# Kernel optimization log

Measured on AMD Instinct MI355X. Metric: run time of the kernel, lower is better.

The kernel has to match this reference:

```python
import jax, jax.numpy as jnp
import numpy as np

B, C, H, W = 16, 512, 32, 32
G = 32            # GroupNorm groups (hard-coded in Normalize)
EPS = 1e-6
TEXT = 180        # text_ch
F = H * W         # in_features, asserted H*W == in_features


def setup_inputs() -> dict:
    key = jax.random.key(0)
    ks = jax.random.split(key, 10)
    s = 0.02
    return {
        "x": jax.random.normal(ks[0], (B, C, H, W), dtype=jnp.float32),
        "condition": jax.random.normal(ks[1], (B, TEXT), dtype=jnp.float32),
        "gamma": jnp.ones((C,), dtype=jnp.float32),
        "beta": jnp.zeros((C,), dtype=jnp.float32),
        "wq": jax.random.normal(ks[2], (C, C), dtype=jnp.float32) * s,   # 1x1 conv [out,in]
        "bq": jax.random.normal(ks[3], (C,), dtype=jnp.float32) * s,
        "wk": jax.random.normal(ks[4], (F, TEXT), dtype=jnp.float32) * s,  # Linear(text_ch -> in_features)
        "bk": jax.random.normal(ks[5], (F,), dtype=jnp.float32) * s,
        "wv": jax.random.normal(ks[6], (F, TEXT), dtype=jnp.float32) * s,
        "bv": jax.random.normal(ks[7], (F,), dtype=jnp.float32) * s,
        "wo": jax.random.normal(ks[8], (C, C), dtype=jnp.float32) * s,   # proj_out 1x1 conv
        "bo": jax.random.normal(ks[9], (C,), dtype=jnp.float32) * s,
    }


def _group_norm(x, gamma, beta):
    b, c, h, w = x.shape
    xg = x.reshape(b, G, c // G, h, w)
    mu = xg.mean(axis=(2, 3, 4), keepdims=True)
    var = xg.var(axis=(2, 3, 4), keepdims=True)
    xn = ((xg - mu) * jax.lax.rsqrt(var + EPS)).reshape(b, c, h, w)
    return xn * gamma[None, :, None, None] + beta[None, :, None, None]


def reference(x, condition, gamma, beta, wq, bq, wk, bk, wv, bv, wo, bo):
    h_ = _group_norm(x, gamma, beta)                       # [B,C,H,W]
    # q: 1x1 conv
    q = jnp.einsum('bchw,oc->bohw', h_, wq) + bq[None, :, None, None]
    # condition.reshape(B,1,-1).repeat(1,C,1)
    cond = jnp.broadcast_to(condition[:, None, :], (B, C, TEXT))  # [B,C,T]
    k = jnp.einsum('bct,ft->bcf', cond, wk) + bk           # [B,C,F]
    v = jnp.einsum('bct,ft->bcf', cond, wv) + bv           # [B,C,F]
    q3 = q.reshape(B, C, H * W).transpose(0, 2, 1)         # [B,N,C], N=HW
    scale = C ** (-0.5)
    attn = jax.nn.softmax(jnp.einsum('bnc,bcf->bnf', q3, k) * scale, axis=2)  # [B,N,F]
    h2 = jnp.einsum('bcf,bnf->bcn', v, attn).reshape(B, C, H, W)
    out = jnp.einsum('bchw,oc->bohw', h2, wo) + bo[None, :, None, None]
    return x + out
```

## Files before the change

### kernel.cpp

```cpp
#include <hip/hip_runtime.h>

#define B_   16
#define C_   512
#define N_   1024
#define F_   1024
#define T_   180
#define G_   32

#define WS_MU    0
#define WS_RSIG  512
#define WS_K     1024
#define WS_V     (1024 + 16384)
#define WS_WQS   (1024 + 2*16384)
#define WS_WOS   (WS_WQS + 512)
#define WS_BQS   (WS_WOS + 512)

__global__ __launch_bounds__(256) void k_prep(
    const float* __restrict__ x, const float* __restrict__ cond,
    const float* __restrict__ wq, const float* __restrict__ bq,
    const float* __restrict__ wk, const float* __restrict__ bk,
    const float* __restrict__ wv, const float* __restrict__ bv,
    const float* __restrict__ wo, float* __restrict__ ws)
{
    const int blk = blockIdx.x;
    const int tid = threadIdx.x;

    if (blk < 512) {
        const float4* xv = (const float4*)(x + (size_t)blk * 16384);
        float s = 0.f, sq = 0.f;
        #pragma unroll
        for (int j = 0; j < 16; ++j) {
            float4 p = xv[tid + (j << 8)];
            s  += (p.x + p.y) + (p.z + p.w);
            sq += p.x * p.x + p.y * p.y + p.z * p.z + p.w * p.w;
        }
        #pragma unroll
        for (int off = 32; off; off >>= 1) {
            s  += __shfl_down(s,  off, 64);
            sq += __shfl_down(sq, off, 64);
        }
        __shared__ float rs[4], rq[4];
        if ((tid & 63) == 0) { rs[tid >> 6] = s; rq[tid >> 6] = sq; }
        __syncthreads();
        if (tid == 0) {
            float S1 = rs[0] + rs[1] + rs[2] + rs[3];
            float S2 = rq[0] + rq[1] + rq[2] + rq[3];
            float mu = S1 * (1.f / 16384.f);
            float var = S2 * (1.f / 16384.f) - mu * mu;
            ws[WS_MU + blk]   = mu;
            ws[WS_RSIG + blk] = rsqrtf(var + 1e-6f);
        }
    } else if (blk < 576) {
        const int idx = blk - 512;
        const int b   = idx >> 2;
        const int f   = ((idx & 3) << 8) + tid;
        __shared__ float condl[T_];
        if (tid < T_) condl[tid] = cond[b * T_ + tid];
        __syncthreads();
        float accK = bk[f];
        float accV = bv[f];
        const float* wkr = wk + f * T_;
        const float* wvr = wv + f * T_;
        #pragma unroll 4
        for (int t = 0; t < T_; ++t) {
            float cf = condl[t];
            accK += cf * wkr[t];
            accV += cf * wvr[t];
        }
        ws[WS_K + b * F_ + f] = accK;
        ws[WS_V + b * F_ + f] = accV;
    } else if (blk < 578) {
        const int c = ((blk - 576) << 8) + tid;
        float acc = 0.f;
        for (int o = 0; o < C_; ++o) acc += wq[o * C_ + c];
        ws[WS_WQS + c] = acc;
    } else if (blk < 580) {
        const int o = ((blk - 578) << 8) + tid;
        const float4* row = (const float4*)(wo + o * C_);
        float acc = 0.f;
        #pragma unroll 8
        for (int j = 0; j < 128; ++j) {
            float4 p = row[j];
            acc += (p.x + p.y) + (p.z + p.w);
        }
        ws[WS_WOS + o] = acc;
    } else {
        float p = bq[tid] + bq[tid + 256];
        #pragma unroll
        for (int off = 32; off; off >>= 1) p += __shfl_down(p, off, 64);
        __shared__ float rb[4];
        if ((tid & 63) == 0) rb[tid >> 6] = p;
        __syncthreads();
        if (tid == 0) ws[WS_BQS] = rb[0] + rb[1] + rb[2] + rb[3];
    }
}

__global__ __launch_bounds__(256) void k_fused(
    const float* __restrict__ x, const float* __restrict__ gamma,
    const float* __restrict__ beta, const float* __restrict__ bo,
    const float* __restrict__ ws, float* __restrict__ out)
{
    const int b   = blockIdx.x >> 5;
    const int n0  = (blockIdx.x & 31) << 5;
    const int tid = threadIdx.x;

    __shared__ float coef[C_];
    __shared__ float KV[2 * F_];
    __shared__ float part[8][32];
    __shared__ float pse[8][32], psv[8][32];
    __shared__ float Sl[32], Al[32];
    __shared__ float opw[4], redmx[4], redmn[4];

    float op = 0.f;
    #pragma unroll
    for (int c = tid; c < C_; c += 256) {
        const int g = c >> 4;
        float rsig = ws[WS_RSIG + b * G_ + g];
        float mu   = ws[WS_MU   + b * G_ + g];
        float gm   = gamma[c];
        float wqs  = ws[WS_WQS + c];
        coef[c] = rsig * gm * wqs;
        op += (beta[c] - mu * rsig * gm) * wqs;
    }
    const float* Kg = ws + WS_K + b * F_;
    const float* Vg = ws + WS_V + b * F_;
    float mx = -1e30f, mn = 1e30f;
    #pragma unroll
    for (int i = tid; i < F_; i += 256) {
        float kv = Kg[i];
        KV[2 * i]     = kv;
        KV[2 * i + 1] = Vg[i];
        mx = fmaxf(mx, kv);
        mn = fminf(mn, kv);
    }
    #pragma unroll
    for (int off = 32; off; off >>= 1) {
        op += __shfl_down(op, off, 64);
        mx = fmaxf(mx, __shfl_down(mx, off, 64));
        mn = fminf(mn, __shfl_down(mn, off, 64));
    }
    if ((tid & 63) == 0) {
        opw[tid >> 6]   = op;
        redmx[tid >> 6] = mx;
        redmn[tid >> 6] = mn;
    }
    __syncthreads();
    const float offset = ws[WS_BQS] + opw[0] + opw[1] + opw[2] + opw[3];
    const float maxK = fmaxf(fmaxf(redmx[0], redmx[1]), fmaxf(redmx[2], redmx[3]));
    const float minK = fminf(fminf(redmn[0], redmn[1]), fminf(redmn[2], redmn[3]));

    const int nl = tid & 31;
    const int cq = tid >> 5;
    {
        const float* xp = x + (((b * C_ + (cq << 6)) << 10) + n0 + nl);
        float acc = 0.f;
        #pragma unroll 8
        for (int ci = 0; ci < 64; ++ci) {
            acc += xp[ci << 10] * coef[(cq << 6) + ci];
        }
        part[cq][nl] = acc;
    }
    __syncthreads();
    if (tid < 32) {
        float s8 = 0.f;
        #pragma unroll
        for (int j = 0; j < 8; ++j) s8 += part[j][tid];
        Sl[tid] = s8 + offset;
    }
    __syncthreads();

    const float LOG2E = 1.4426950408889634f;
    const float scale = 0.044194173824159216f;
    const float s  = Sl[nl] * scale;
    const float sl = s * LOG2E;
    const float ml = (s >= 0.f ? maxK : minK) * sl;

    float se = 0.f, sv = 0.f;
    const int fq = tid >> 5;
    const int fbase = fq << 7;
    #pragma unroll 8
    for (int fi = 0; fi < 128; ++fi) {
        const int f = fbase + fi;
        float kf = KV[2 * f];
        float vf = KV[2 * f + 1];
        float e = exp2f(fmaf(sl, kf, -ml));
        se += e;
        sv = fmaf(vf, e, sv);
    }
    pse[fq][nl] = se;
    psv[fq][nl] = sv;
    __syncthreads();
    if (tid < 32) {
        float den = 0.f, num = 0.f;
        #pragma unroll
        for (int j = 0; j < 8; ++j) { den += pse[j][tid]; num += psv[j][tid]; }
        Al[tid] = num / den;
    }
    __syncthreads();

    const int col = tid & 7;
    const int row = tid >> 3;
    float av[4];
    #pragma unroll
    for (int j = 0; j < 4; ++j) av[j] = Al[(col << 2) + j];
    const float* WOS = ws + WS_WOS;

    for (int p = 0; p < 16; ++p) {
        const int o = (p << 5) + row;
        const float w   = WOS[o];
        const float bof = bo[o];
        const size_t base = (((size_t)(b * C_ + o)) << 10) + n0 + (col << 2);
        float4 xv = *(const float4*)(x + base);
        float4 ov;
        ov.x = xv.x + fmaf(av[0], w, bof);
        ov.y = xv.y + fmaf(av[1], w, bof);
        ov.z = xv.z + fmaf(av[2], w, bof);
        ov.w = xv.w + fmaf(av[3], w, bof);
        *(float4*)(out + base) = ov;
    }
}

extern "C" void kernel_launch(void* const* d_in, const int* in_sizes, int n_in,
                              void* d_out, int out_size, void* d_ws, size_t ws_size,
                              hipStream_t stream) {
    const float* x     = (const float*)d_in[0];
    const float* cond  = (const float*)d_in[1];
    const float* gamma = (const float*)d_in[2];
    const float* beta  = (const float*)d_in[3];
    const float* wq    = (const float*)d_in[4];
    const float* bq    = (const float*)d_in[5];
    const float* wk    = (const float*)d_in[6];
    const float* bk    = (const float*)d_in[7];
    const float* wv    = (const float*)d_in[8];
    const float* bv    = (const float*)d_in[9];
    const float* wo    = (const float*)d_in[10];
    const float* bo    = (const float*)d_in[11];
    float* ws  = (float*)d_ws;
    float* out = (float*)d_out;

    hipLaunchKernelGGL(k_prep, dim3(581), dim3(256), 0, stream,
                       x, cond, wq, bq, wk, bk, wv, bv, wo, ws);
    hipLaunchKernelGGL(k_fused, dim3(512), dim3(256), 0, stream,
                       x, gamma, beta, bo, ws, out);
}
```

Measured before the change: 138.3 us.

## Fuse group-norm stats with per-group q-projection partial sums in one x pass

The previous flow read x once in the prep kernel for group statistics, again in the fused kernel for the q dot product, and a third time for the residual. Now a new kernel computes group mean/rstd and the weighted channel sum per group in the same read of x, writing per-group partial q values to workspace. The fused kernel then sums 32 group partials instead of re-reading 512 channels of x. It also processes 64 positions per block with fewer blocks. The cost is an extra launch and a serialized dependency: the weight-prep kernel must finish before k_gs, since k_gs reads its column sums of wq.

```diff
diff --git a/kernel.cpp b/kernel.cpp
--- a/kernel.cpp
+++ b/kernel.cpp
@@ -7,16 +7,15 @@
 #define T_   180
 #define G_   32
 
-#define WS_MU    0
-#define WS_RSIG  512
-#define WS_K     1024
-#define WS_V     (1024 + 16384)
-#define WS_WQS   (1024 + 2*16384)
+#define WS_K     0
+#define WS_V     16384
+#define WS_WQS   (2*16384)
 #define WS_WOS   (WS_WQS + 512)
 #define WS_BQS   (WS_WOS + 512)
-
-__global__ __launch_bounds__(256) void k_prep(
-    const float* __restrict__ x, const float* __restrict__ cond,
+#define WS_SG    (WS_BQS + 64)
+
+__global__ __launch_bounds__(256) void k_w(
+    const float* __restrict__ cond,
     const float* __restrict__ wq, const float* __restrict__ bq,
     const float* __restrict__ wk, const float* __restrict__ bk,
     const float* __restrict__ wv, const float* __restrict__ bv,
@@ -25,35 +24,9 @@
     const int blk = blockIdx.x;
     const int tid = threadIdx.x;
 
-    if (blk < 512) {
-        const float4* xv = (const float4*)(x + (size_t)blk * 16384);
-        float s = 0.f, sq = 0.f;
-        #pragma unroll
-        for (int j = 0; j < 16; ++j) {
-            float4 p = xv[tid + (j << 8)];
-            s  += (p.x + p.y) + (p.z + p.w);
-            sq += p.x * p.x + p.y * p.y + p.z * p.z + p.w * p.w;
-        }
-        #pragma unroll
-        for (int off = 32; off; off >>= 1) {
-            s  += __shfl_down(s,  off, 64);
-            sq += __shfl_down(sq, off, 64);
-        }
-        __shared__ float rs[4], rq[4];
-        if ((tid & 63) == 0) { rs[tid >> 6] = s; rq[tid >> 6] = sq; }
-        __syncthreads();
-        if (tid == 0) {
-            float S1 = rs[0] + rs[1] + rs[2] + rs[3];
-            float S2 = rq[0] + rq[1] + rq[2] + rq[3];
-            float mu = S1 * (1.f / 16384.f);
-            float var = S2 * (1.f / 16384.f) - mu * mu;
-            ws[WS_MU + blk]   = mu;
-            ws[WS_RSIG + blk] = rsqrtf(var + 1e-6f);
-        }
-    } else if (blk < 576) {
-        const int idx = blk - 512;
-        const int b   = idx >> 2;
-        const int f   = ((idx & 3) << 8) + tid;
+    if (blk < 64) {
+        const int b = blk >> 2;
+        const int f = ((blk & 3) << 8) + tid;
         __shared__ float condl[T_];
         if (tid < T_) condl[tid] = cond[b * T_ + tid];
         __syncthreads();
@@ -69,13 +42,13 @@
         }
         ws[WS_K + b * F_ + f] = accK;
         ws[WS_V + b * F_ + f] = accV;
-    } else if (blk < 578) {
-        const int c = ((blk - 576) << 8) + tid;
+    } else if (blk < 66) {
+        const int c = ((blk - 64) << 8) + tid;
         float acc = 0.f;
         for (int o = 0; o < C_; ++o) acc += wq[o * C_ + c];
         ws[WS_WQS + c] = acc;
-    } else if (blk < 580) {
-        const int o = ((blk - 578) << 8) + tid;
+    } else if (blk < 68) {
+        const int o = ((blk - 66) << 8) + tid;
         const float4* row = (const float4*)(wo + o * C_);
         float acc = 0.f;
         #pragma unroll 8
@@ -95,33 +68,81 @@
     }
 }
 
+__global__ __launch_bounds__(256) void k_gs(
+    const float* __restrict__ x, const float* __restrict__ gamma,
+    const float* __restrict__ beta, float* __restrict__ ws)
+{
+    const int blk = blockIdx.x;
+    const int tid = threadIdx.x;
+
+    __shared__ float wl[16], bl[16];
+    __shared__ float rs[4], rq[4];
+    __shared__ float muS, rsigS;
+
+    if (tid < 16) {
+        const int c = ((blk & 31) << 4) + tid;
+        float wqs = ws[WS_WQS + c];
+        wl[tid] = gamma[c] * wqs;
+        bl[tid] = beta[c] * wqs;
+    }
+    __syncthreads();
+
+    const float4* xv = (const float4*)(x + (size_t)blk * 16384);
+    float s = 0.f, sq = 0.f;
+    float4 acc = make_float4(0.f, 0.f, 0.f, 0.f);
+    #pragma unroll
+    for (int c = 0; c < 16; ++c) {
+        float4 p = xv[(c << 8) + tid];
+        s  += (p.x + p.y) + (p.z + p.w);
+        sq += p.x * p.x + p.y * p.y + p.z * p.z + p.w * p.w;
+        float w = wl[c];
+        acc.x += p.x * w; acc.y += p.y * w; acc.z += p.z * w; acc.w += p.w * w;
+    }
+    #pragma unroll
+    for (int off = 32; off; off >>= 1) {
+        s  += __shfl_down(s,  off, 64);
+        sq += __shfl_down(sq, off, 64);
+    }
+    if ((tid & 63) == 0) { rs[tid >> 6] = s; rq[tid >> 6] = sq; }
+    __syncthreads();
+    if (tid == 0) {
+        float S1 = rs[0] + rs[1] + rs[2] + rs[3];
+        float S2 = rq[0] + rq[1] + rq[2] + rq[3];
+        float mu = S1 * (1.f / 16384.f);
+        float var = S2 * (1.f / 16384.f) - mu * mu;
+        muS = mu;
+        rsigS = rsqrtf(var + 1e-6f);
+    }
+    __syncthreads();
+
+    float G1 = 0.f, G2 = 0.f;
+    #pragma unroll
+    for (int j = 0; j < 16; ++j) { G1 += wl[j]; G2 += bl[j]; }
+    const float rsig = rsigS;
+    const float off0 = G2 - rsig * muS * G1;
+
+    float4 sg;
+    sg.x = rsig * acc.x + off0;
+    sg.y = rsig * acc.y + off0;
+    sg.z = rsig * acc.z + off0;
+    sg.w = rsig * acc.w + off0;
+    ((float4*)(ws + WS_SG + (size_t)blk * N_))[tid] = sg;
+}
+
 __global__ __launch_bounds__(256) void k_fused(
-    const float* __restrict__ x, const float* __restrict__ gamma,
-    const float* __restrict__ beta, const float* __restrict__ bo,
+    const float* __restrict__ x, const float* __restrict__ bo,
     const float* __restrict__ ws, float* __restrict__ out)
 {
-    const int b   = blockIdx.x >> 5;
-    const int n0  = (blockIdx.x & 31) << 5;
+    const int b   = blockIdx.x >> 4;
+    const int n0  = (blockIdx.x & 15) << 6;
     const int tid = threadIdx.x;
 
-    __shared__ float coef[C_];
     __shared__ float KV[2 * F_];
-    __shared__ float part[8][32];
-    __shared__ float pse[8][32], psv[8][32];
-    __shared__ float Sl[32], Al[32];
-    __shared__ float opw[4], redmx[4], redmn[4];
-
-    float op = 0.f;
-    #pragma unroll
-    for (int c = tid; c < C_; c += 256) {
-        const int g = c >> 4;
-        float rsig = ws[WS_RSIG + b * G_ + g];
-        float mu   = ws[WS_MU   + b * G_ + g];
-        float gm   = gamma[c];
-        float wqs  = ws[WS_WQS + c];
-        coef[c] = rsig * gm * wqs;
-        op += (beta[c] - mu * rsig * gm) * wqs;
-    }
+    __shared__ float ps[4][64];
+    __shared__ float pse[4][64], psv[4][64];
+    __shared__ float Sl[64], Al[64];
+    __shared__ float redmx[4], redmn[4];
+
     const float* Kg = ws + WS_K + b * F_;
     const float* Vg = ws + WS_V + b * F_;
     float mx = -1e30f, mn = 1e30f;
@@ -135,39 +156,27 @@
     }
     #pragma unroll
     for (int off = 32; off; off >>= 1) {
-        op += __shfl_down(op, off, 64);
         mx = fmaxf(mx, __shfl_down(mx, off, 64));
         mn = fminf(mn, __shfl_down(mn, off, 64));
     }
-    if ((tid & 63) == 0) {
-        opw[tid >> 6]   = op;
-        redmx[tid >> 6] = mx;
-        redmn[tid >> 6] = mn;
-    }
-    __syncthreads();
-    const float offset = ws[WS_BQS] + opw[0] + opw[1] + opw[2] + opw[3];
+    if ((tid & 63) == 0) { redmx[tid >> 6] = mx; redmn[tid >> 6] = mn; }
+
+    const int nl = tid & 63, qq = tid >> 6;
+    {
+        const float* sgp = ws + WS_SG + ((size_t)(b * G_ + (qq << 3)) << 10) + n0 + nl;
+        float p = 0.f;
+        #pragma unroll
+        for (int j = 0; j < 8; ++j) p += sgp[(size_t)j << 10];
+        ps[qq][nl] = p;
+    }
+    __syncthreads();
+    if (tid < 64) {
+        Sl[tid] = ws[WS_BQS] + ps[0][tid] + ps[1][tid] + ps[2][tid] + ps[3][tid];
+    }
+    __syncthreads();
+
     const float maxK = fmaxf(fmaxf(redmx[0], redmx[1]), fmaxf(redmx[2], redmx[3]));
     const float minK = fminf(fminf(redmn[0], redmn[1]), fminf(redmn[2], redmn[3]));
-
-    const int nl = tid & 31;
-    const int cq = tid >> 5;
-    {
-        const float* xp = x + (((b * C_ + (cq << 6)) << 10) + n0 + nl);
-        float acc = 0.f;
-        #pragma unroll 8
-        for (int ci = 0; ci < 64; ++ci) {
-            acc += xp[ci << 10] * coef[(cq << 6) + ci];
-        }
-        part[cq][nl] = acc;
-    }
-    __syncthreads();
-    if (tid < 32) {
-        float s8 = 0.f;
-        #pragma unroll
-        for (int j = 0; j < 8; ++j) s8 += part[j][tid];
-        Sl[tid] = s8 + offset;
-    }
-    __syncthreads();
 
     const float LOG2E = 1.4426950408889634f;
     const float scale = 0.044194173824159216f;
@@ -176,10 +185,9 @@
     const float ml = (s >= 0.f ? maxK : minK) * sl;
 
     float se = 0.f, sv = 0.f;
-    const int fq = tid >> 5;
-    const int fbase = fq << 7;
+    const int fbase = qq << 8;
     #pragma unroll 8
-    for (int fi = 0; fi < 128; ++fi) {
+    for (int fi = 0; fi < 256; ++fi) {
         const int f = fbase + fi;
         float kf = KV[2 * f];
         float vf = KV[2 * f + 1];
@@ -187,26 +195,25 @@
         se += e;
         sv = fmaf(vf, e, sv);
     }
-    pse[fq][nl] = se;
-    psv[fq][nl] = sv;
-    __syncthreads();
-    if (tid < 32) {
-        float den = 0.f, num = 0.f;
-        #pragma unroll
-        for (int j = 0; j < 8; ++j) { den += pse[j][tid]; num += psv[j][tid]; }
+    pse[qq][nl] = se;
+    psv[qq][nl] = sv;
+    __syncthreads();
+    if (tid < 64) {
+        float den = pse[0][tid] + pse[1][tid] + pse[2][tid] + pse[3][tid];
+        float num = psv[0][tid] + psv[1][tid] + psv[2][tid] + psv[3][tid];
         Al[tid] = num / den;
     }
     __syncthreads();
 
-    const int col = tid & 7;
-    const int row = tid >> 3;
+    const int col = tid & 15;
+    const int row = tid >> 4;
     float av[4];
     #pragma unroll
     for (int j = 0; j < 4; ++j) av[j] = Al[(col << 2) + j];
     const float* WOS = ws + WS_WOS;
 
-    for (int p = 0; p < 16; ++p) {
-        const int o = (p << 5) + row;
+    for (int p = 0; p < 32; ++p) {
+        const int o = (p << 4) + row;
         const float w   = WOS[o];
         const float bof = bo[o];
         const size_t base = (((size_t)(b * C_ + o)) << 10) + n0 + (col << 2);
@@ -238,8 +245,10 @@
     float* ws  = (float*)d_ws;
     float* out = (float*)d_out;
 
-    hipLaunchKernelGGL(k_prep, dim3(581), dim3(256), 0, stream,
-                       x, cond, wq, bq, wk, bk, wv, bv, wo, ws);
-    hipLaunchKernelGGL(k_fused, dim3(512), dim3(256), 0, stream,
-                       x, gamma, beta, bo, ws, out);
-}
+    hipLaunchKernelGGL(k_w, dim3(69), dim3(256), 0, stream,
+                       cond, wq, bq, wk, bk, wv, bv, wo, ws);
+    hipLaunchKernelGGL(k_gs, dim3(512), dim3(256), 0, stream,
+                       x, gamma, beta, ws);
+    hipLaunchKernelGGL(k_fused, dim3(256), dim3(256), 0, stream,
+                       x, bo, ws, out);
+}
```

Result: slower. 141.9 us (+2.6%).
